# Optimization experiments

Hardware: AMD Instinct MI355X
Metric: run time of the kernel (lower is better)

## Reference

```python
import jax, jax.numpy as jnp
import numpy as np

NUM_EMB = 512
EMB_DIM = 64

def conv1d(x, w, b=None, stride=1, padding=0):
    # x: (N,C,L), w: (O,I,K) torch Conv1d layout
    out = jax.lax.conv_general_dilated(x, w, (stride,), [(padding, padding)],
                                       dimension_numbers=('NCH', 'OIH', 'NCH'))
    if b is not None:
        out = out + b[None, :, None]
    return out

def conv_transpose1d(x, w, b, stride, padding):
    # w: (I,O,K) torch ConvTranspose1d layout -> flip kernel, swap I/O
    k = w.shape[2]
    wf = jnp.flip(w, 2).transpose(1, 0, 2)  # (O,I,K)
    pad = k - 1 - padding
    out = jax.lax.conv_general_dilated(x, wf, (1,), [(pad, pad)],
                                       lhs_dilation=(stride,),
                                       dimension_numbers=('NCH', 'OIH', 'NCH'))
    return out + b[None, :, None]

def residual_block(x, w1, w2):
    # ReLU -> conv3(pad1, no bias) -> ReLU -> conv1(no bias), residual add
    h = conv1d(jax.nn.relu(x), w1, None, 1, 1)
    h = conv1d(jax.nn.relu(h), w2, None, 1, 0)
    return x + h

def residual_stack(x, r0_w1, r0_w2, r1_w1, r1_w2):
    x = residual_block(x, r0_w1, r0_w2)
    x = residual_block(x, r1_w1, r1_w2)
    return jax.nn.relu(x)

def vq(z, emb):
    # z: (B, C=64, T); torch VectorQuantizerEMA eval path (decay=0, not training)
    B, C, T = z.shape
    inputs = z.transpose(0, 2, 1)                 # (B,T,C)
    flat = inputs.reshape(-1, C)                  # (B*T, C)
    d = (jnp.sum(flat * flat, axis=1, keepdims=True)
         + jnp.sum(emb * emb, axis=1)
         - 2.0 * flat @ emb.T)                    # (B*T, K)
    idx = jnp.argmin(d, axis=1)
    enc = jax.nn.one_hot(idx, NUM_EMB, dtype=flat.dtype)  # (B*T, K)
    q = (enc @ emb).reshape(B, T, C)
    # straight-through estimator
    q = inputs + jax.lax.stop_gradient(q - inputs)
    return q.transpose(0, 2, 1)                   # (B,C,T)

def reference(x, enc_w1, enc_b1, enc_w2, enc_b2, enc_w3, enc_b3,
              enc_r0_w1, enc_r0_w2, enc_r1_w1, enc_r1_w2,
              prevq_w, prevq_b, emb,
              dec_w1, dec_b1, dec_r0_w1, dec_r0_w2, dec_r1_w1, dec_r1_w2,
              dect1_w, dect1_b, dect2_w, dect2_b):
    # Encoder
    h = jax.nn.relu(conv1d(x, enc_w1, enc_b1, 2, 1))
    h = jax.nn.relu(conv1d(h, enc_w2, enc_b2, 2, 1))
    h = conv1d(h, enc_w3, enc_b3, 1, 1)
    h = residual_stack(h, enc_r0_w1, enc_r0_w2, enc_r1_w1, enc_r1_w2)
    # pre-VQ 1x1 conv
    z = conv1d(h, prevq_w, prevq_b, 1, 0)
    # Vector quantization
    q = vq(z, emb)
    # Decoder
    d = conv1d(q, dec_w1, dec_b1, 1, 1)
    d = residual_stack(d, dec_r0_w1, dec_r0_w2, dec_r1_w1, dec_r1_w2)
    d = jax.nn.relu(conv_transpose1d(d, dect1_w, dect1_b, 2, 1))
    return conv_transpose1d(d, dect2_w, dect2_b, 2, 1)

def setup_inputs() -> dict:
    key = jax.random.key(0)
    ks = jax.random.split(key, 25)
    def n(k, shape, s=0.05):
        return jax.random.normal(k, shape, dtype=jnp.float32) * s
    return {
        'x': jax.random.normal(ks[0], (16, 768, 4096), dtype=jnp.float32),
        'enc_w1': n(ks[1], (32, 768, 4)), 'enc_b1': n(ks[2], (32,)),
        'enc_w2': n(ks[3], (64, 32, 4)), 'enc_b2': n(ks[4], (64,)),
        'enc_w3': n(ks[5], (64, 64, 3)), 'enc_b3': n(ks[6], (64,)),
        'enc_r0_w1': n(ks[7], (32, 64, 3)), 'enc_r0_w2': n(ks[8], (64, 32, 1)),
        'enc_r1_w1': n(ks[9], (32, 64, 3)), 'enc_r1_w2': n(ks[10], (64, 32, 1)),
        'prevq_w': n(ks[11], (64, 64, 1)), 'prevq_b': n(ks[12], (64,)),
        'emb': jax.random.normal(ks[13], (512, 64), dtype=jnp.float32),
        'dec_w1': n(ks[14], (64, 64, 3)), 'dec_b1': n(ks[15], (64,)),
        'dec_r0_w1': n(ks[16], (32, 64, 3)), 'dec_r0_w2': n(ks[17], (64, 32, 1)),
        'dec_r1_w1': n(ks[18], (32, 64, 3)), 'dec_r1_w2': n(ks[19], (64, 32, 1)),
        'dect1_w': n(ks[20], (64, 32, 4)), 'dect1_b': n(ks[21], (32,)),
        'dect2_w': n(ks[22], (32, 64, 4)), 'dect2_b': n(ks[23], (64,)),
    }
```

## Files before the change

kernel.cpp:

```cpp
#include <hip/hip_runtime.h>


typedef _Float16 half8 __attribute__((ext_vector_type(8)));
typedef float f32x4 __attribute__((ext_vector_type(4)));
union H8u { half8 h; int4 i; };
union P4u { _Float16 e[4]; int2 u; };

__device__ __forceinline__ void splitf(float v, _Float16& h, _Float16& l) {
  h = (_Float16)v; l = (_Float16)((v - (float)h) * 2048.0f);
}
#define INV2048 (1.0f / 2048.0f)

#define OFF_C1   0
#define OFF_C2   98304
#define OFF_C3   106496
#define OFF_ER0A 122880
#define OFF_ER0B 131072
#define OFF_ER1A 133120
#define OFF_ER1B 141312
#define OFF_PQ   143360
#define OFF_DW1  147456
#define OFF_DR0A 163840
#define OFF_DR0B 172032
#define OFF_DR1A 174080
#define OFF_DR1B 182272
#define OFF_T1   184320
#define OFF_T2   200704
#define WTOT     217088

struct WPtrs {
  const float *c1, *c2, *c3, *er0a, *er0b, *er1a, *er1b, *pq,
              *dw1, *dr0a, *dr0b, *dr1a, *dr1b, *t1, *t2;
};

__device__ __forceinline__ int tpose_kt(int par, int tap) {
  if (par == 0) { if (tap == 0) return 3; if (tap == 1) return 1; }
  else          { if (tap == 1) return 2; if (tap == 2) return 0; }
  return -1;
}

__global__ __launch_bounds__(256) void prep_k(WPtrs P, _Float16* __restrict__ WH,
                                              _Float16* __restrict__ WL) {
  int s = blockIdx.x * 256 + threadIdx.x;
  if (s >= WTOT) return;
  float v = 0.f;
  if (s < OFF_C2) {
    int t = s, co = t / 3072, kk = t % 3072;
    v = P.c1[(co * 768 + (kk >> 2)) * 4 + (kk & 3)];
  } else if (s < OFF_C3) {
    int t = s - OFF_C2, co = t >> 7, kk = t & 127;
    v = P.c2[(co * 32 + (kk >> 2)) * 4 + (kk & 3)];
  } else if (s < OFF_ER0A) {
    int t = s - OFF_C3, co = t >> 8, kk = t & 255, tap = kk & 3;
    if (tap < 3) v = P.c3[(co * 64 + (kk >> 2)) * 3 + tap];
  } else if (s < OFF_ER0B) {
    int t = s - OFF_ER0A, co = t >> 8, kk = t & 255, tap = kk & 3;
    if (tap < 3) v = P.er0a[(co * 64 + (kk >> 2)) * 3 + tap];
  } else if (s < OFF_ER1A) {
    int t = s - OFF_ER0B; v = P.er0b[t];
  } else if (s < OFF_ER1B) {
    int t = s - OFF_ER1A, co = t >> 8, kk = t & 255, tap = kk & 3;
    if (tap < 3) v = P.er1a[(co * 64 + (kk >> 2)) * 3 + tap];
  } else if (s < OFF_PQ) {
    int t = s - OFF_ER1B; v = P.er1b[t];
  } else if (s < OFF_DW1) {
    int t = s - OFF_PQ; v = P.pq[t];
  } else if (s < OFF_DR0A) {
    int t = s - OFF_DW1, co = t >> 8, kk = t & 255, tap = kk & 3;
    if (tap < 3) v = P.dw1[(co * 64 + (kk >> 2)) * 3 + tap];
  } else if (s < OFF_DR0B) {
    int t = s - OFF_DR0A, co = t >> 8, kk = t & 255, tap = kk & 3;
    if (tap < 3) v = P.dr0a[(co * 64 + (kk >> 2)) * 3 + tap];
  } else if (s < OFF_DR1A) {
    int t = s - OFF_DR0B; v = P.dr0b[t];
  } else if (s < OFF_DR1B) {
    int t = s - OFF_DR1A, co = t >> 8, kk = t & 255, tap = kk & 3;
    if (tap < 3) v = P.dr1a[(co * 64 + (kk >> 2)) * 3 + tap];
  } else if (s < OFF_T1) {
    int t = s - OFF_DR1B; v = P.dr1b[t];
  } else if (s < OFF_T2) {
    int t = s - OFF_T1, nn = t >> 8, kk = t & 255;
    int par = nn >> 5, co = nn & 31, ci = kk >> 2;
    int kt = tpose_kt(par, kk & 3);
    if (kt >= 0) v = P.t1[(ci * 32 + co) * 4 + kt];
  } else {
    int t = s - OFF_T2, nn = t >> 7, kk = t & 127;
    int par = nn >> 6, co = nn & 63, ci = kk >> 2;
    int kt = tpose_kt(par, kk & 3);
    if (kt >= 0) v = P.t2[(ci * 64 + co) * 4 + kt];
  }
  _Float16 h, l; splitf(v, h, l);
  WH[s] = h; WL[s] = l;
}

__global__ __launch_bounds__(256, 2) void conv1_k(
    const float* __restrict__ x, const _Float16* __restrict__ WH,
    const _Float16* __restrict__ WL, float* __restrict__ Pout, int cchunks) {
  const int tid = threadIdx.x;
  const int w = tid >> 6, lane = tid & 63, lm = lane & 15, quad = lane >> 4;
  const int m0 = blockIdx.x * 64, n = blockIdx.y, kpart = blockIdx.z;
  const int mrow = m0 + w * 16 + lm;
  const int pbase = 2 * mrow - 1;
  const bool lo = pbase >= 0;
  const bool hi = pbase + 3 <= 4095;
  const int pc0 = lo ? pbase : 1;
  const int pc3 = hi ? pbase + 3 : pbase + 1;
  const float* xn = x + (size_t)n * 768 * 4096;
  const float* xq = xn + (size_t)(quad * 2) * 4096;
  const _Float16* bh0 = WH + (size_t)lm * 3072 + quad * 8;
  const _Float16* bl0 = WL + (size_t)lm * 3072 + quad * 8;
  const _Float16* bh1 = bh0 + 16 * 3072;
  const _Float16* bl1 = bl0 + 16 * 3072;
  f32x4 acc1[2], acc2[2];
#pragma unroll
  for (int j = 0; j < 2; ++j)
#pragma unroll
    for (int r = 0; r < 4; ++r) { acc1[j][r] = 0.f; acc2[j][r] = 0.f; }

  const int c0 = kpart * cchunks;
#pragma unroll 1
  for (int cc = 0; cc < cchunks; ++cc) {
    const int c = c0 + cc;
    const float* rpc = xq + (size_t)c * 32 * 4096;
    const int kb = c * 128;
#pragma unroll
    for (int ks = 0; ks < 4; ++ks) {
      const float* r0 = rpc + (size_t)ks * 8 * 4096;
      const float* r1 = r0 + 4096;
      float  t0  = r0[pc0];
      float2 v0m = *(const float2*)(r0 + pbase + 1);
      float  t3  = r0[pc3];
      float  u0  = r1[pc0];
      float2 v1m = *(const float2*)(r1 + pbase + 1);
      float  u3  = r1[pc3];
      H8u b0h, b0l, b1h, b1l;
      b0h.i = *(const int4*)(bh0 + kb + ks * 32);
      b0l.i = *(const int4*)(bl0 + kb + ks * 32);
      b1h.i = *(const int4*)(bh1 + kb + ks * 32);
      b1l.i = *(const int4*)(bl1 + kb + ks * 32);
      float a[8];
      a[0] = lo ? t0 : 0.f; a[1] = v0m.x; a[2] = v0m.y; a[3] = hi ? t3 : 0.f;
      a[4] = lo ? u0 : 0.f; a[5] = v1m.x; a[6] = v1m.y; a[7] = hi ? u3 : 0.f;
      H8u ah, al;
#pragma unroll
      for (int e = 0; e < 8; ++e) {
        _Float16 h, l; splitf(a[e], h, l);
        ah.h[e] = h; al.h[e] = l;
      }
      acc1[0] = __builtin_amdgcn_mfma_f32_16x16x32_f16(ah.h, b0h.h, acc1[0], 0, 0, 0);
      acc2[0] = __builtin_amdgcn_mfma_f32_16x16x32_f16(ah.h, b0l.h, acc2[0], 0, 0, 0);
      acc2[0] = __builtin_amdgcn_mfma_f32_16x16x32_f16(al.h, b0h.h, acc2[0], 0, 0, 0);
      acc1[1] = __builtin_amdgcn_mfma_f32_16x16x32_f16(ah.h, b1h.h, acc1[1], 0, 0, 0);
      acc2[1] = __builtin_amdgcn_mfma_f32_16x16x32_f16(ah.h, b1l.h, acc2[1], 0, 0, 0);
      acc2[1] = __builtin_amdgcn_mfma_f32_16x16x32_f16(al.h, b1h.h, acc2[1], 0, 0, 0);
    }
  }
#pragma unroll
  for (int j = 0; j < 2; ++j) {
    int col = j * 16 + lm;
    float4 o;
    o.x = acc1[j][0] + acc2[j][0] * INV2048;
    o.y = acc1[j][1] + acc2[j][1] * INV2048;
    o.z = acc1[j][2] + acc2[j][2] * INV2048;
    o.w = acc1[j][3] + acc2[j][3] * INV2048;
    *(float4*)(Pout + (size_t)kpart * (16 * 32 * 2048)
               + ((size_t)n * 32 + col) * 2048 + m0 + w * 16 + quad * 4) = o;
  }
}

template<int CI, int KP, int NT, int STRIDE,
         bool RELU_IN, bool RELU_OUT, bool BIAS, bool TPOSE, bool RESBLK,
         bool PSUM = false>
__global__ __launch_bounds__(256) void gconv(
    const float* __restrict__ in, const _Float16* __restrict__ WH,
    const _Float16* __restrict__ WL, const float* __restrict__ bias,
    const _Float16* __restrict__ W2H, const _Float16* __restrict__ W2L,
    float* __restrict__ out, int Lin, int Lout,
    const float* __restrict__ inbias, int nparts, int pplane) {
  constexpr int CP = 32 * STRIDE + 4;
  constexpr int CP4 = CP / 4;
  constexpr int AP = KP + 8;
  constexpr int KS = KP / 32;
  constexpr int NTW = (NT == 2) ? 1 : NT / 2;
  __shared__ float xs[CI * CP];
  __shared__ _Float16 Ah[32 * AP];
  __shared__ _Float16 Al[32 * AP];
  __shared__ _Float16 A2h[RESBLK ? 32 * 40 : 1];
  __shared__ _Float16 A2l[RESBLK ? 32 * 40 : 1];
  const int tid = threadIdx.x;
  const int w = tid >> 6, lane = tid & 63, lm = lane & 15, quad = lane >> 4;
  const int mt = w >> 1, ntb = (w & 1) * NTW;
  const int m0 = blockIdx.x * 32, n = blockIdx.y;
  const int base = m0 * STRIDE - 1;
  const float* inN = in + (size_t)n * CI * Lin;
  constexpr int SLOTS = CI * CP4;
#pragma unroll
  for (int it = 0; it < (SLOTS + 255) / 256; ++it) {
    int idx = it * 256 + tid;
    if (idx < SLOTS) {
      int row = idx / CP4, c4 = idx % CP4;
      int p0 = base + c4 * 4;
      const float* rp = inN + (size_t)row * Lin;
      float4 v;
      if (PSUM) {
        v.x = 0.f; v.y = 0.f; v.z = 0.f; v.w = 0.f;
        bool i0 = (p0   >= 0 && p0   < Lin);
        bool i1 = (p0+1 >= 0 && p0+1 < Lin);
        bool i2 = (p0+2 >= 0 && p0+2 < Lin);
        bool i3 = (p0+3 >= 0 && p0+3 < Lin);
        bool full = (p0 >= 0 && p0 + 3 < Lin);
        for (int p = 0; p < nparts; ++p) {
          const float* rpp = rp + (size_t)p * pplane;
          if (full) {
            float4 t = *(const float4*)(rpp + p0);
            v.x += t.x; v.y += t.y; v.z += t.z; v.w += t.w;
          } else {
            if (i0) v.x += rpp[p0];
            if (i1) v.y += rpp[p0+1];
            if (i2) v.z += rpp[p0+2];
            if (i3) v.w += rpp[p0+3];
          }
        }
        float bv = inbias[row];
        v.x = i0 ? fmaxf(v.x + bv, 0.f) : 0.f;
        v.y = i1 ? fmaxf(v.y + bv, 0.f) : 0.f;
        v.z = i2 ? fmaxf(v.z + bv, 0.f) : 0.f;
        v.w = i3 ? fmaxf(v.w + bv, 0.f) : 0.f;
      } else {
        if (p0 >= 0 && p0 + 3 < Lin) v = *(const float4*)(rp + p0);
        else {
          v.x = (p0   >= 0 && p0   < Lin) ? rp[p0]   : 0.f;
          v.y = (p0+1 >= 0 && p0+1 < Lin) ? rp[p0+1] : 0.f;
          v.z = (p0+2 >= 0 && p0+2 < Lin) ? rp[p0+2] : 0.f;
          v.w = (p0+3 >= 0 && p0+3 < Lin) ? rp[p0+3] : 0.f;
        }
      }
      *(float4*)(&xs[row * CP + c4 * 4]) = v;
    }
  }
  __syncthreads();
#pragma unroll
  for (int it = 0; it < (32 * CI) / 256; ++it) {
    int slot = it * 256 + tid;
    int ci = slot & (CI - 1), m = slot / CI;
    const float* xr = &xs[ci * CP + STRIDE * m];
    float a0 = xr[0], a1 = xr[1], a2 = xr[2], a3 = xr[3];
    if (RELU_IN) { a0 = fmaxf(a0,0.f); a1 = fmaxf(a1,0.f);
                   a2 = fmaxf(a2,0.f); a3 = fmaxf(a3,0.f); }
    P4u ph, pl;
    splitf(a0, ph.e[0], pl.e[0]); splitf(a1, ph.e[1], pl.e[1]);
    splitf(a2, ph.e[2], pl.e[2]); splitf(a3, ph.e[3], pl.e[3]);
    *(int2*)(&Ah[m * AP + ci * 4]) = ph.u;
    *(int2*)(&Al[m * AP + ci * 4]) = pl.u;
  }
  __syncthreads();
  f32x4 acc1[NTW], acc2[NTW];
#pragma unroll
  for (int j = 0; j < NTW; ++j)
#pragma unroll
    for (int r = 0; r < 4; ++r) { acc1[j][r] = 0.f; acc2[j][r] = 0.f; }
  H8u bh[2][NTW], bl[2][NTW];
#pragma unroll
  for (int j = 0; j < NTW; ++j) {
    int col = (ntb + j) * 16 + lm;
    bh[0][j].i = *(const int4*)(WH + (size_t)col * KP + quad * 8);
    bl[0][j].i = *(const int4*)(WL + (size_t)col * KP + quad * 8);
  }
#pragma unroll
  for (int ks = 0; ks < KS; ++ks) {
    int cur = ks & 1;
    if (ks + 1 < KS) {
#pragma unroll
      for (int j = 0; j < NTW; ++j) {
        int col = (ntb + j) * 16 + lm;
        bh[cur ^ 1][j].i = *(const int4*)(WH + (size_t)col * KP + (ks+1) * 32 + quad * 8);
        bl[cur ^ 1][j].i = *(const int4*)(WL + (size_t)col * KP + (ks+1) * 32 + quad * 8);
      }
    }
    H8u ah, al;
    ah.i = *(const int4*)(&Ah[(mt * 16 + lm) * AP + ks * 32 + quad * 8]);
    al.i = *(const int4*)(&Al[(mt * 16 + lm) * AP + ks * 32 + quad * 8]);
#pragma unroll
    for (int j = 0; j < NTW; ++j) {
      acc1[j] = __builtin_amdgcn_mfma_f32_16x16x32_f16(ah.h, bh[cur][j].h, acc1[j], 0,0,0);
      acc2[j] = __builtin_amdgcn_mfma_f32_16x16x32_f16(ah.h, bl[cur][j].h, acc2[j], 0,0,0);
      acc2[j] = __builtin_amdgcn_mfma_f32_16x16x32_f16(al.h, bh[cur][j].h, acc2[j], 0,0,0);
    }
  }
  if (RESBLK) {
    int co2 = (w & 1) * 16 + lm;
#pragma unroll
    for (int r = 0; r < 4; ++r) {
      float hv = fmaxf(acc1[0][r] + acc2[0][r] * INV2048, 0.f);
      _Float16 hh, hl; splitf(hv, hh, hl);
      int m = mt * 16 + quad * 4 + r;
      A2h[m * 40 + co2] = hh; A2l[m * 40 + co2] = hl;
    }
    __syncthreads();
    f32x4 c1[2], c2[2];
#pragma unroll
    for (int j = 0; j < 2; ++j)
#pragma unroll
      for (int r = 0; r < 4; ++r) { c1[j][r] = 0.f; c2[j][r] = 0.f; }
    H8u a2h, a2l;
    a2h.i = *(const int4*)(&A2h[(mt * 16 + lm) * 40 + quad * 8]);
    a2l.i = *(const int4*)(&A2l[(mt * 16 + lm) * 40 + quad * 8]);
    int ntb2 = (w & 1) * 2;
#pragma unroll
    for (int j = 0; j < 2; ++j) {
      int col = (ntb2 + j) * 16 + lm;
      H8u wbh, wbl;
      wbh.i = *(const int4*)(W2H + col * 32 + quad * 8);
      wbl.i = *(const int4*)(W2L + col * 32 + quad * 8);
      c1[j] = __builtin_amdgcn_mfma_f32_16x16x32_f16(a2h.h, wbh.h, c1[j], 0,0,0);
      c2[j] = __builtin_amdgcn_mfma_f32_16x16x32_f16(a2h.h, wbl.h, c2[j], 0,0,0);
      c2[j] = __builtin_amdgcn_mfma_f32_16x16x32_f16(a2l.h, wbh.h, c2[j], 0,0,0);
    }
#pragma unroll
    for (int j = 0; j < 2; ++j) {
      int col = (ntb2 + j) * 16 + lm;
      float4 o;
#pragma unroll
      for (int r = 0; r < 4; ++r) {
        int m = mt * 16 + quad * 4 + r;
        float res = xs[col * CP + m + 1];
        ((float*)&o)[r] = res + c1[j][r] + c2[j][r] * INV2048;
      }
      *(float4*)(out + ((size_t)n * 64 + col) * Lout + m0 + mt * 16 + quad * 4) = o;
    }
  } else {
    constexpr int CO = TPOSE ? NT * 8 : NT * 16;
#pragma unroll
    for (int j = 0; j < NTW; ++j) {
      int col = (ntb + j) * 16 + lm;
      int par = TPOSE ? (col / CO) : 0;
      int co  = TPOSE ? (col % CO) : col;
      float bv = BIAS ? bias[co] : 0.f;
      float vr[4];
#pragma unroll
      for (int r = 0; r < 4; ++r) {
        float v = acc1[j][r] + acc2[j][r] * INV2048 + bv;
        vr[r] = RELU_OUT ? fmaxf(v, 0.f) : v;
      }
      if (TPOSE) {
#pragma unroll
        for (int r = 0; r < 4; ++r) {
          int m = m0 + mt * 16 + quad * 4 + r;
          out[((size_t)n * CO + co) * Lout + 2 * m + par] = vr[r];
        }
      } else {
        float4 o; o.x = vr[0]; o.y = vr[1]; o.z = vr[2]; o.w = vr[3];
        *(float4*)(out + ((size_t)n * CO + co) * Lout + m0 + mt * 16 + quad * 4) = o;
      }
    }
  }
}

__global__ void enorm_k(const float* __restrict__ emb, float* __restrict__ en) {
  int e = blockIdx.x * blockDim.x + threadIdx.x;
  if (e >= 512) return;
  float s = 0.f;
  const float* r = emb + (size_t)e * 64;
  for (int c = 0; c < 64; ++c) s = fmaf(r[c], r[c], s);
  en[e] = s;
}

__global__ __launch_bounds__(256) void vq_fused(
    const float* __restrict__ sIn, const _Float16* __restrict__ PQH,
    const _Float16* __restrict__ PQL, const float* __restrict__ pqb,
    const float* __restrict__ emb, const float* __restrict__ en,
    float* __restrict__ q) {
  __shared__ float xs[64 * 68];
  __shared__ _Float16 Ah[64 * 72];
  __shared__ _Float16 Al[64 * 72];
  __shared__ float zl[64 * 65];
  __shared__ float dred[4 * 64];
  __shared__ int   ired[4 * 64];
  __shared__ int   idxs[64];
  const int tid = threadIdx.x;
  const int w = tid >> 6, lane = tid & 63, lm = lane & 15, quad = lane >> 4;
  const int n = blockIdx.y, t0 = blockIdx.x * 64;
#pragma unroll
  for (int it = 0; it < 4; ++it) {
    int idx = it * 256 + tid;
    int row = idx >> 4, c4 = idx & 15;
    float4 v = *(const float4*)(sIn + ((size_t)n * 64 + row) * 1024 + t0 + c4 * 4);
    *(float4*)(&xs[row * 68 + c4 * 4]) = v;
  }
  __syncthreads();
#pragma unroll
  for (int it = 0; it < 16; ++it) {
    int slot = it * 256 + tid;
    int ci = slot & 63, t = slot >> 6;
    float v = fmaxf(xs[ci * 68 + t], 0.f);
    _Float16 h, l; splitf(v, h, l);
    Ah[t * 72 + ci] = h; Al[t * 72 + ci] = l;
  }
  __syncthreads();
  f32x4 a1[4], a2[4];
#pragma unroll
  for (int j = 0; j < 4; ++j)
#pragma unroll
    for (int r = 0; r < 4; ++r) { a1[j][r] = 0.f; a2[j][r] = 0.f; }
#pragma unroll
  for (int ks = 0; ks < 2; ++ks) {
    H8u ah, al;
    ah.i = *(const int4*)(&Ah[(w * 16 + lm) * 72 + ks * 32 + quad * 8]);
    al.i = *(const int4*)(&Al[(w * 16 + lm) * 72 + ks * 32 + quad * 8]);
#pragma unroll
    for (int j = 0; j < 4; ++j) {
      int col = j * 16 + lm;
      H8u bh, bl;
      bh.i = *(const int4*)(PQH + col * 64 + ks * 32 + quad * 8);
      bl.i = *(const int4*)(PQL + col * 64 + ks * 32 + quad * 8);
      a1[j] = __builtin_amdgcn_mfma_f32_16x16x32_f16(ah.h, bh.h, a1[j], 0,0,0);
      a2[j] = __builtin_amdgcn_mfma_f32_16x16x32_f16(ah.h, bl.h, a2[j], 0,0,0);
      a2[j] = __builtin_amdgcn_mfma_f32_16x16x32_f16(al.h, bh.h, a2[j], 0,0,0);
    }
  }
#pragma unroll
  for (int j = 0; j < 4; ++j) {
    int col = j * 16 + lm;
    float bv = pqb[col];
#pragma unroll
    for (int r = 0; r < 4; ++r) {
      int t = w * 16 + quad * 4 + r;
      zl[t * 65 + col] = a1[j][r] + a2[j][r] * INV2048 + bv;
    }
  }
  __syncthreads();
  int tt = tid & 63, cq = tid >> 6;
  float zv[64];
#pragma unroll
  for (int c = 0; c < 64; ++c) zv[c] = zl[tt * 65 + c];
  float best = 1e30f; int bidx = 0;
  for (int e = cq * 128; e < cq * 128 + 128; ++e) {
    const float* er = emb + (size_t)e * 64;
    float dot = 0.f;
#pragma unroll
    for (int c = 0; c < 64; ++c) dot = fmaf(zv[c], er[c], dot);
    float d = en[e] - 2.f * dot;
    if (d < best) { best = d; bidx = e; }
  }
  dred[cq * 64 + tt] = best;
  ired[cq * 64 + tt] = bidx;
  __syncthreads();
  if (cq == 0) {
    for (int j = 1; j < 4; ++j) {
      float d = dred[j * 64 + tt]; int i2 = ired[j * 64 + tt];
      if (d < best || (d == best && i2 < bidx)) { best = d; bidx = i2; }
    }
    idxs[tt] = bidx;
  }
  __syncthreads();
  for (int it = 0; it < 16; ++it) {
    int c = cq * 16 + it;
    q[((size_t)n * 64 + c) * 1024 + t0 + tt] = emb[(size_t)idxs[tt] * 64 + c];
  }
}

extern "C" void kernel_launch(void* const* d_in, const int* in_sizes, int n_in,
                              void* d_out, int out_size, void* d_ws, size_t ws_size,
                              hipStream_t stream) {
  const float* x        = (const float*)d_in[0];
  const float* enc_b1   = (const float*)d_in[2];
  const float* enc_b2   = (const float*)d_in[4];
  const float* enc_b3   = (const float*)d_in[6];
  const float* prevq_b  = (const float*)d_in[12];
  const float* emb      = (const float*)d_in[13];
  const float* dec_b1   = (const float*)d_in[15];
  const float* dect1_b  = (const float*)d_in[21];
  const float* dect2_b  = (const float*)d_in[23];
  float* out = (float*)d_out;

  WPtrs P;
  P.c1  = (const float*)d_in[1];  P.c2  = (const float*)d_in[3];
  P.c3  = (const float*)d_in[5];  P.er0a = (const float*)d_in[7];
  P.er0b = (const float*)d_in[8]; P.er1a = (const float*)d_in[9];
  P.er1b = (const float*)d_in[10]; P.pq = (const float*)d_in[11];
  P.dw1 = (const float*)d_in[14]; P.dr0a = (const float*)d_in[16];
  P.dr0b = (const float*)d_in[17]; P.dr1a = (const float*)d_in[18];
  P.dr1b = (const float*)d_in[19]; P.t1 = (const float*)d_in[20];
  P.t2  = (const float*)d_in[22];

  float* A  = (float*)d_ws;
  float* B  = A + (1u << 20);
  float* EN = B + (1u << 20);
  _Float16* WH = (_Float16*)(EN + 1024);
  _Float16* WL = WH + WTOT;
  float* PP = (float*)(WL + WTOT);

  const size_t baseBytes = (size_t)((char*)PP - (char*)d_ws);
  const size_t planeB = (size_t)16 * 32 * 2048 * 4;
  int nparts = 1;
  float* Pbuf = A;
  if (ws_size >= baseBytes + 4 * planeB) { nparts = 4; Pbuf = PP; }
  else if (ws_size >= baseBytes + 2 * planeB) { nparts = 2; Pbuf = PP; }

  dim3 blk(256);
  prep_k<<<dim3((WTOT + 255) / 256), blk, 0, stream>>>(P, WH, WL);
  enorm_k<<<dim3(2), blk, 0, stream>>>(emb, EN);
  conv1_k<<<dim3(32, 16, nparts), blk, 0, stream>>>(x, WH + OFF_C1, WL + OFF_C1,
                                                    Pbuf, 24 / nparts);
  gconv<32,128,4,2, false,true,true, false,false, true><<<dim3(32,16), blk, 0, stream>>>(
      Pbuf, WH+OFF_C2, WL+OFF_C2, enc_b2, nullptr, nullptr, B, 2048, 1024,
      enc_b1, nparts, 16 * 32 * 2048);
  gconv<64,256,4,1, false,false,true, false,false><<<dim3(32,16), blk, 0, stream>>>(
      B, WH+OFF_C3, WL+OFF_C3, enc_b3, nullptr, nullptr, A, 1024, 1024,
      nullptr, 1, 0);
  gconv<64,256,2,1, true,false,false, false,true><<<dim3(32,16), blk, 0, stream>>>(
      A, WH+OFF_ER0A, WL+OFF_ER0A, nullptr, WH+OFF_ER0B, WL+OFF_ER0B, B, 1024, 1024,
      nullptr, 1, 0);
  gconv<64,256,2,1, true,false,false, false,true><<<dim3(32,16), blk, 0, stream>>>(
      B, WH+OFF_ER1A, WL+OFF_ER1A, nullptr, WH+OFF_ER1B, WL+OFF_ER1B, A, 1024, 1024,
      nullptr, 1, 0);
  vq_fused<<<dim3(16,16), blk, 0, stream>>>(A, WH+OFF_PQ, WL+OFF_PQ, prevq_b, emb, EN, B);
  gconv<64,256,4,1, false,false,true, false,false><<<dim3(32,16), blk, 0, stream>>>(
      B, WH+OFF_DW1, WL+OFF_DW1, dec_b1, nullptr, nullptr, A, 1024, 1024,
      nullptr, 1, 0);
  gconv<64,256,2,1, true,false,false, false,true><<<dim3(32,16), blk, 0, stream>>>(
      A, WH+OFF_DR0A, WL+OFF_DR0A, nullptr, WH+OFF_DR0B, WL+OFF_DR0B, B, 1024, 1024,
      nullptr, 1, 0);
  gconv<64,256,2,1, true,false,false, false,true><<<dim3(32,16), blk, 0, stream>>>(
      B, WH+OFF_DR1A, WL+OFF_DR1A, nullptr, WH+OFF_DR1B, WL+OFF_DR1B, A, 1024, 1024,
      nullptr, 1, 0);
  gconv<64,256,4,1, true,true,true, true,false><<<dim3(32,16), blk, 0, stream>>>(
      A, WH+OFF_T1, WL+OFF_T1, dect1_b, nullptr, nullptr, B, 1024, 2048,
      nullptr, 1, 0);
  gconv<32,128,8,1, false,false,true, true,false><<<dim3(64,16), blk, 0, stream>>>(
      B, WH+OFF_T2, WL+OFF_T2, dect2_b, nullptr, nullptr, out, 2048, 4096,
      nullptr, 1, 0);
}
```

Baseline: 633.2 us.

## Stage conv1 input through double-buffered LDS with coalesced float4 loads

The first encoder conv now loads 16-channel slabs of the input with coalesced float4 global reads. It splits them into fp16 hi/lo once and writes them into double-buffered shared memory, and the MFMA fragments are read back from LDS. The next chunk's global load overlaps the current chunk's compute. This replaces the old per-lane strided scalar and float2 loads, where each input value was fetched and split redundantly. Launch bounds rise to 6 blocks per CU, which adds LDS use, a barrier per chunk and more register pressure.

```diff
diff --git a/kernel.cpp b/kernel.cpp
--- a/kernel.cpp
+++ b/kernel.cpp
@@ -93,68 +93,100 @@
   WH[s] = h; WL[s] = l;
 }
 
-__global__ __launch_bounds__(256, 2) void conv1_k(
+__global__ __launch_bounds__(256, 6) void conv1_k(
     const float* __restrict__ x, const _Float16* __restrict__ WH,
-    const _Float16* __restrict__ WL, float* __restrict__ Pout, int cchunks) {
+    const _Float16* __restrict__ WL, float* __restrict__ Pout, int cpp) {
+  __shared__ _Float16 Hs[2][16 * 136];
+  __shared__ _Float16 Ls[2][16 * 136];
   const int tid = threadIdx.x;
   const int w = tid >> 6, lane = tid & 63, lm = lane & 15, quad = lane >> 4;
   const int m0 = blockIdx.x * 64, n = blockIdx.y, kpart = blockIdx.z;
-  const int mrow = m0 + w * 16 + lm;
-  const int pbase = 2 * mrow - 1;
-  const bool lo = pbase >= 0;
-  const bool hi = pbase + 3 <= 4095;
-  const int pc0 = lo ? pbase : 1;
-  const int pc3 = hi ? pbase + 3 : pbase + 1;
+  const int r = w * 16 + lm;
+  const int pb = 2 * m0 - 1;
   const float* xn = x + (size_t)n * 768 * 4096;
-  const float* xq = xn + (size_t)(quad * 2) * 4096;
+  const int r0s = tid / 33, c0s = tid % 33;
+  const int r1s = (256 + tid) / 33, c1s = (256 + tid) % 33;
+  const int r2s = (512 + tid) / 33, c2s = (512 + tid) % 33;
   const _Float16* bh0 = WH + (size_t)lm * 3072 + quad * 8;
   const _Float16* bl0 = WL + (size_t)lm * 3072 + quad * 8;
   const _Float16* bh1 = bh0 + 16 * 3072;
   const _Float16* bl1 = bl0 + 16 * 3072;
+
   f32x4 acc1[2], acc2[2];
 #pragma unroll
   for (int j = 0; j < 2; ++j)
 #pragma unroll
-    for (int r = 0; r < 4; ++r) { acc1[j][r] = 0.f; acc2[j][r] = 0.f; }
-
-  const int c0 = kpart * cchunks;
+    for (int rr = 0; rr < 4; ++rr) { acc1[j][rr] = 0.f; acc2[j][rr] = 0.f; }
+
+  const int cb0 = kpart * cpp;
+  float4 sv0, sv1, sv2;
+
+#define C1_LD1(SV, RS, CS) { \
+    int p0 = pb + 4 * (CS); \
+    const float* rp = xn + (size_t)(chb + (RS)) * 4096; \
+    if (p0 >= 0 && p0 + 3 < 4096) SV = *(const float4*)(rp + p0); \
+    else { \
+      SV.x = (p0   >= 0 && p0   < 4096) ? rp[p0]   : 0.f; \
+      SV.y = (p0+1 >= 0 && p0+1 < 4096) ? rp[p0+1] : 0.f; \
+      SV.z = (p0+2 >= 0 && p0+2 < 4096) ? rp[p0+2] : 0.f; \
+      SV.w = (p0+3 >= 0 && p0+3 < 4096) ? rp[p0+3] : 0.f; } }
+
+#define C1_LOAD(cc) { \
+    int chb = (cb0 + (cc)) * 16; \
+    C1_LD1(sv0, r0s, c0s) \
+    C1_LD1(sv1, r1s, c1s) \
+    if (tid < 16) C1_LD1(sv2, r2s, c2s) }
+
+#define C1_WR1(SV, RS, CS, B) { \
+    P4u ph, pl; \
+    splitf(SV.x, ph.e[0], pl.e[0]); splitf(SV.y, ph.e[1], pl.e[1]); \
+    splitf(SV.z, ph.e[2], pl.e[2]); splitf(SV.w, ph.e[3], pl.e[3]); \
+    *(int2*)(&Hs[B][(RS) * 136 + 4 * (CS)]) = ph.u; \
+    *(int2*)(&Ls[B][(RS) * 136 + 4 * (CS)]) = pl.u; }
+
+#define C1_WRITE(B) { \
+    C1_WR1(sv0, r0s, c0s, B) \
+    C1_WR1(sv1, r1s, c1s, B) \
+    if (tid < 16) C1_WR1(sv2, r2s, c2s, B) }
+
+#define C1_COMP(cc, B) { \
+    const uint* Hdw = (const uint*)(&Hs[B][0]); \
+    const uint* Ldw = (const uint*)(&Ls[B][0]); \
+    const int kkb = ((cb0 + (cc)) * 64); \
+    _Pragma("unroll") \
+    for (int ks = 0; ks < 2; ++ks) { \
+      const int ci0 = ks * 8 + quad * 2; \
+      const int bse = ci0 * 68 + r; \
+      H8u ah, al; \
+      ah.i.x = Hdw[bse];      ah.i.y = Hdw[bse + 1]; \
+      ah.i.z = Hdw[bse + 68]; ah.i.w = Hdw[bse + 69]; \
+      al.i.x = Ldw[bse];      al.i.y = Ldw[bse + 1]; \
+      al.i.z = Ldw[bse + 68]; al.i.w = Ldw[bse + 69]; \
+      H8u b0h, b0l, b1h, b1l; \
+      b0h.i = *(const int4*)(bh0 + kkb + ks * 32); \
+      b0l.i = *(const int4*)(bl0 + kkb + ks * 32); \
+      b1h.i = *(const int4*)(bh1 + kkb + ks * 32); \
+      b1l.i = *(const int4*)(bl1 + kkb + ks * 32); \
+      acc1[0] = __builtin_amdgcn_mfma_f32_16x16x32_f16(ah.h, b0h.h, acc1[0], 0,0,0); \
+      acc2[0] = __builtin_amdgcn_mfma_f32_16x16x32_f16(ah.h, b0l.h, acc2[0], 0,0,0); \
+      acc2[0] = __builtin_amdgcn_mfma_f32_16x16x32_f16(al.h, b0h.h, acc2[0], 0,0,0); \
+      acc1[1] = __builtin_amdgcn_mfma_f32_16x16x32_f16(ah.h, b1h.h, acc1[1], 0,0,0); \
+      acc2[1] = __builtin_amdgcn_mfma_f32_16x16x32_f16(ah.h, b1l.h, acc2[1], 0,0,0); \
+      acc2[1] = __builtin_amdgcn_mfma_f32_16x16x32_f16(al.h, b1h.h, acc2[1], 0,0,0); \
+    } }
+
+  C1_LOAD(0);
+  C1_WRITE(0);
+  __syncthreads();
 #pragma unroll 1
-  for (int cc = 0; cc < cchunks; ++cc) {
-    const int c = c0 + cc;
-    const float* rpc = xq + (size_t)c * 32 * 4096;
-    const int kb = c * 128;
-#pragma unroll
-    for (int ks = 0; ks < 4; ++ks) {
-      const float* r0 = rpc + (size_t)ks * 8 * 4096;
-      const float* r1 = r0 + 4096;
-      float  t0  = r0[pc0];
-      float2 v0m = *(const float2*)(r0 + pbase + 1);
-      float  t3  = r0[pc3];
-      float  u0  = r1[pc0];
-      float2 v1m = *(const float2*)(r1 + pbase + 1);
-      float  u3  = r1[pc3];
-      H8u b0h, b0l, b1h, b1l;
-      b0h.i = *(const int4*)(bh0 + kb + ks * 32);
-      b0l.i = *(const int4*)(bl0 + kb + ks * 32);
-      b1h.i = *(const int4*)(bh1 + kb + ks * 32);
-      b1l.i = *(const int4*)(bl1 + kb + ks * 32);
-      float a[8];
-      a[0] = lo ? t0 : 0.f; a[1] = v0m.x; a[2] = v0m.y; a[3] = hi ? t3 : 0.f;
-      a[4] = lo ? u0 : 0.f; a[5] = v1m.x; a[6] = v1m.y; a[7] = hi ? u3 : 0.f;
-      H8u ah, al;
-#pragma unroll
-      for (int e = 0; e < 8; ++e) {
-        _Float16 h, l; splitf(a[e], h, l);
-        ah.h[e] = h; al.h[e] = l;
-      }
-      acc1[0] = __builtin_amdgcn_mfma_f32_16x16x32_f16(ah.h, b0h.h, acc1[0], 0, 0, 0);
-      acc2[0] = __builtin_amdgcn_mfma_f32_16x16x32_f16(ah.h, b0l.h, acc2[0], 0, 0, 0);
-      acc2[0] = __builtin_amdgcn_mfma_f32_16x16x32_f16(al.h, b0h.h, acc2[0], 0, 0, 0);
-      acc1[1] = __builtin_amdgcn_mfma_f32_16x16x32_f16(ah.h, b1h.h, acc1[1], 0, 0, 0);
-      acc2[1] = __builtin_amdgcn_mfma_f32_16x16x32_f16(ah.h, b1l.h, acc2[1], 0, 0, 0);
-      acc2[1] = __builtin_amdgcn_mfma_f32_16x16x32_f16(al.h, b1h.h, acc2[1], 0, 0, 0);
-    }
-  }
+  for (int cc = 0; cc < cpp; ++cc) {
+    const int cur = cc & 1;
+    if (cc + 1 < cpp) C1_LOAD(cc + 1);
+    C1_COMP(cc, cur);
+    if (cc + 1 < cpp) C1_WRITE(cur ^ 1);
+    __syncthreads();
+  }
+
 #pragma unroll
   for (int j = 0; j < 2; ++j) {
     int col = j * 16 + lm;
@@ -166,6 +198,11 @@
     *(float4*)(Pout + (size_t)kpart * (16 * 32 * 2048)
                + ((size_t)n * 32 + col) * 2048 + m0 + w * 16 + quad * 4) = o;
   }
+#undef C1_LD1
+#undef C1_LOAD
+#undef C1_WR1
+#undef C1_WRITE
+#undef C1_COMP
 }
 
 template<int CI, int KP, int NT, int STRIDE,
@@ -501,7 +538,7 @@
   prep_k<<<dim3((WTOT + 255) / 256), blk, 0, stream>>>(P, WH, WL);
   enorm_k<<<dim3(2), blk, 0, stream>>>(emb, EN);
   conv1_k<<<dim3(32, 16, nparts), blk, 0, stream>>>(x, WH + OFF_C1, WL + OFF_C1,
-                                                    Pbuf, 24 / nparts);
+                                                    Pbuf, 48 / nparts);
   gconv<32,128,4,2, false,true,true, false,false, true><<<dim3(32,16), blk, 0, stream>>>(
       Pbuf, WH+OFF_C2, WL+OFF_C2, enc_b2, nullptr, nullptr, B, 2048, 1024,
       enc_b1, nparts, 16 * 32 * 2048);
```

Result: slower. 687.7 us (+8.6%).
